# Kernel optimization log

Hardware: AMD Instinct MI355X
Metric: run time of the kernel (lower is better)

## Reference

```python
import jax, jax.numpy as jnp
import numpy as np

D = 256        # in_dim == out_dim for both node types
NH = 8         # n_heads
DH = D // NH   # d_over_h = 32
NA = 50000     # nodes of type 'a'
NB = 20000     # nodes of type 'b'
E = 100000     # edges per edge type
MAX_LEN = 27759
LN_EPS = 1e-5


def _rte_table():
    # Fixed (non-trainable) sinusoidal table from RelativeTemporalEncoding
    pos = np.arange(MAX_LEN, dtype=np.float32)[:, None]
    div = np.exp(np.arange(0, D, 2, dtype=np.float32) * (-np.log(10000.0) / D))
    tab = np.zeros((MAX_LEN, D), dtype=np.float32)
    tab[:, 0::2] = np.sin(pos * div) / np.sqrt(D)
    tab[:, 1::2] = np.cos(pos * div) / np.sqrt(D)
    return jnp.asarray(tab)


def setup_inputs() -> dict:
    key = jax.random.key(0)
    ks = jax.random.split(key, 24)
    s = 1.0 / np.sqrt(D)
    sh = 1.0 / np.sqrt(DH)
    inp = {
        "Ha": jax.random.normal(ks[0], (NA, D), jnp.float32),
        "Hb": jax.random.normal(ks[1], (NB, D), jnp.float32),
        "rte_emb": _rte_table(),
        # stacked per-node-type weights, index 0 -> 'a', 1 -> 'b'; torch Linear layout [out, in]
        "Wq": jax.random.normal(ks[2], (2, D, D), jnp.float32) * s,
        "Wk": jax.random.normal(ks[3], (2, D, D), jnp.float32) * s,
        "Wm": jax.random.normal(ks[4], (2, D, D), jnp.float32) * s,
        "Wa": jax.random.normal(ks[5], (2, D, D), jnp.float32) * s,
        "rteW": jax.random.normal(ks[6], (2, D, D), jnp.float32) * s,
        "rteb": jnp.zeros((2, D), jnp.float32),
        "ln_g": jnp.ones((2, D), jnp.float32),
        "ln_b": jnp.zeros((2, D), jnp.float32),
        "res_alpha": jnp.ones((2,), jnp.float32),
        # stacked per-edge-type params, index 0 -> e1 (a->a), 1 -> e2 (b->a), 2 -> e3 (a->b)
        "Watt": jax.random.normal(ks[7], (3, DH, DH), jnp.float32) * sh,
        "Wmsg": jax.random.normal(ks[8], (3, DH, DH), jnp.float32) * sh,
        "prior": jnp.ones((3,), jnp.float32),
        "src1": jax.random.randint(ks[9], (E,), 0, NA, jnp.int32),
        "dst1": jax.random.randint(ks[10], (E,), 0, NA, jnp.int32),
        "t1": jax.random.randint(ks[11], (E,), 1, MAX_LEN, jnp.int32),
        "src2": jax.random.randint(ks[12], (E,), 0, NB, jnp.int32),
        "dst2": jax.random.randint(ks[13], (E,), 0, NA, jnp.int32),
        "t2": jax.random.randint(ks[14], (E,), 1, MAX_LEN, jnp.int32),
        "src3": jax.random.randint(ks[15], (E,), 0, NA, jnp.int32),
        "dst3": jax.random.randint(ks[16], (E,), 0, NB, jnp.int32),
        "t3": jax.random.randint(ks[17], (E,), 1, MAX_LEN, jnp.int32),
    }
    return inp


def _edge_agg(Hs, Hd, src, dst, t, Wk_s, Wm_s, Wq_t, rW, rb, Wa_e, Wm_e, pr, rte_emb, n_dst):
    """Per-edge-type attention + segment softmax + weighted scatter-sum."""
    ne = src.shape[0]
    # RTE on gathered source features: h_src + Linear(emb[27759 - time])
    hs = Hs[src] + rte_emb[MAX_LEN - t] @ rW.T + rb            # [E, D]
    K = (hs @ Wk_s.T).reshape(ne, NH, DH)                       # [E, H, DH]
    Q = (Hd[dst] @ Wq_t.T).reshape(ne, NH, DH)                  # [E, H, DH]
    att = jnp.einsum('ehd,df,ehf->eh', K, Wa_e, Q) * pr / np.sqrt(DH).astype(np.float32)
    msg = jnp.einsum('ehd,df->ehf', (hs @ Wm_s.T).reshape(ne, NH, DH), Wm_e)
    # segment softmax over destination nodes (DGL mailbox softmax)
    amax = jax.lax.stop_gradient(jax.ops.segment_max(att, dst, num_segments=n_dst))
    ex = jnp.exp(att - amax[dst])
    den = jax.ops.segment_sum(ex, dst, num_segments=n_dst)
    w = ex / den[dst]                                           # [E, H]
    agg = jax.ops.segment_sum(w[..., None] * msg, dst, num_segments=n_dst)  # [N, H, DH]
    cnt = jax.ops.segment_sum(jnp.ones((ne,), jnp.float32), dst, num_segments=n_dst)
    return agg, (cnt > 0).astype(jnp.float32)


def _update(agg, Hx, Wa_n, g, b, ra):
    x = jax.nn.elu(agg.reshape(agg.shape[0], -1)) @ Wa_n.T
    alpha = jax.nn.sigmoid(ra)
    u = alpha * x + (1.0 - alpha) * Hx
    mu = jnp.mean(u, axis=-1, keepdims=True)
    var = jnp.var(u, axis=-1, keepdims=True)
    return (u - mu) / jnp.sqrt(var + LN_EPS) * g + b


def reference(Ha, Hb, rte_emb, Wq, Wk, Wm, Wa, rteW, rteb, ln_g, ln_b, res_alpha,
              Watt, Wmsg, prior, src1, dst1, t1, src2, dst2, t2, src3, dst3, t3):
    # e1: a -> a ; e2: b -> a ; e3: a -> b
    agg1, h1 = _edge_agg(Ha, Ha, src1, dst1, t1, Wk[0], Wm[0], Wq[0], rteW[0], rteb[0], Watt[0], Wmsg[0], prior[0], rte_emb, NA)
    agg2, h2 = _edge_agg(Hb, Ha, src2, dst2, t2, Wk[1], Wm[1], Wq[0], rteW[1], rteb[1], Watt[1], Wmsg[1], prior[1], rte_emb, NA)
    agg3, h3 = _edge_agg(Ha, Hb, src3, dst3, t3, Wk[0], Wm[0], Wq[1], rteW[0], rteb[0], Watt[2], Wmsg[2], prior[2], rte_emb, NB)
    # cross_reducer='mean': average over edge types that delivered messages
    agg_a = (agg1 + agg2) / jnp.maximum(h1 + h2, 1.0)[:, None, None]
    agg_b = agg3 / jnp.maximum(h3, 1.0)[:, None, None]
    out_a = _update(agg_a, Ha, Wa[0], ln_g[0], ln_b[0], res_alpha[0])
    out_b = _update(agg_b, Hb, Wa[1], ln_g[1], ln_b[1], res_alpha[1])
    return (out_a, out_b)
```

## Files before the change

kernel.cpp:

```cpp
#include <hip/hip_runtime.h>
#include <hip/hip_bf16.h>
#include <math.h>

typedef __hip_bfloat16 bf16;
typedef __attribute__((ext_vector_type(8))) short bf16x8v;
typedef __attribute__((ext_vector_type(4))) float f32x4;


__device__ __forceinline__ float eluf(float x) { return x > 0.f ? x : (__expf(x) - 1.f); }
__device__ __forceinline__ float b2f(unsigned short u) { return __uint_as_float((unsigned)u << 16); }
__device__ __forceinline__ unsigned short f2b(float f) {
    unsigned u = __float_as_uint(f);
    return (unsigned short)((u + 0x7fffu + ((u >> 16) & 1u)) >> 16);
}
__device__ __forceinline__ void unpack8(uint4 u, float* o) {
    o[0] = __uint_as_float(u.x << 16); o[1] = __uint_as_float(u.x & 0xffff0000u);
    o[2] = __uint_as_float(u.y << 16); o[3] = __uint_as_float(u.y & 0xffff0000u);
    o[4] = __uint_as_float(u.z << 16); o[5] = __uint_as_float(u.z & 0xffff0000u);
    o[6] = __uint_as_float(u.w << 16); o[7] = __uint_as_float(u.w & 0xffff0000u);
}
__device__ __forceinline__ void unpack4(ushort4 u, float* o) {
    o[0] = b2f(u.x); o[1] = b2f(u.y); o[2] = b2f(u.z); o[3] = b2f(u.w);
}

#define ASYNC_LDS16(g, l) \
    __builtin_amdgcn_global_load_lds((const __attribute__((address_space(1))) void*)(g), \
                                     (__attribute__((address_space(3))) void*)(l), 16, 0, 0)

__global__ void zero_kernel(int* __restrict__ z0, int nz0, int* __restrict__ z1, int nz1)
{
    for (int i = blockIdx.x * 256 + threadIdx.x; i < nz0; i += gridDim.x * 256) z0[i] = 0;
    if (blockIdx.x == 0 && threadIdx.x < (unsigned)nz1) z1[threadIdx.x] = 0;
}

__global__ void conv_fold_hist_kernel(
    const float* s0, bf16* o0, int n0, const float* s1, bf16* o1, int n1,
    const float* s2, bf16* o2, int n2, const float* s3, bf16* o3, int n3,
    const float* s4, bf16* o4, int n4, const float* s5, bf16* o5, int n5,
    const float* __restrict__ Watt, const float* __restrict__ Wmsg,
    const float* __restrict__ prior,
    const float* __restrict__ Wq, const float* __restrict__ Wm,
    bf16* __restrict__ WcatA, bf16* __restrict__ WcatB,
    float* __restrict__ Wmx1f, float* __restrict__ Wmx2f, float* __restrict__ Wmx3f,
    const int* __restrict__ d1, const int* __restrict__ d2, const int* __restrict__ d3,
    int2* __restrict__ m1, int2* __restrict__ m2, int2* __restrict__ m3,
    int E1, int E2, int E3)
{
    const int bid = blockIdx.x;
    if (bid < 3072) {
        const int seg = bid >> 9;
        const int lb = bid & 511;
        const float* sp; bf16* op; int n8;
        switch (seg) {
            case 0: sp = s0; op = o0; n8 = n0; break;
            case 1: sp = s1; op = o1; n8 = n1; break;
            case 2: sp = s2; op = o2; n8 = n2; break;
            case 3: sp = s3; op = o3; n8 = n3; break;
            case 4: sp = s4; op = o4; n8 = n4; break;
            default: sp = s5; op = o5; n8 = n5; break;
        }
        for (int i = lb * 256 + threadIdx.x; i < n8; i += 512 * 256) {
            const float4* p = (const float4*)(sp + (size_t)i * 8);
            float4 a = p[0], b = p[1];
            uint4 u;
            u.x = (unsigned)f2b(a.x) | ((unsigned)f2b(a.y) << 16);
            u.y = (unsigned)f2b(a.z) | ((unsigned)f2b(a.w) << 16);
            u.z = (unsigned)f2b(b.x) | ((unsigned)f2b(b.y) << 16);
            u.w = (unsigned)f2b(b.z) | ((unsigned)f2b(b.w) << 16);
            *(uint4*)(op + (size_t)i * 8) = u;
        }
        return;
    }
    if (bid >= 4608) {
        int i = (bid - 4608) * 256 + threadIdx.x;
        if (i < E1) atomicAdd(&m1[d1[i]].y, 1);
        else if (i < E1 + E2) atomicAdd(&m2[d2[i - E1]].y, 1);
        else if (i < E1 + E2 + E3) atomicAdd(&m3[d3[i - E1 - E2]].y, 1);
        return;
    }
    const int fb = bid - 3072;
    const int g = fb >> 8;
    const int i = fb & 255;
    const int j = threadIdx.x;
    const int h = i >> 5, r = i & 31;
    const float* A; const float* W; float sc = 1.f; int tr = 0;
    bf16* ob; float* of = nullptr;
    const float isq = 0.17677669529663687f;
    switch (g) {
        case 0: A = Watt;        sc = prior[0] * isq; W = Wq;         ob = WcatA;                       break;
        case 1: A = Watt + 1024; sc = prior[1] * isq; W = Wq;         ob = WcatA + (size_t)256 * 256;   break;
        case 2: A = Watt + 2048; sc = prior[2] * isq; W = Wq + 65536; ob = WcatB;                       break;
        case 3: A = Wmsg;        tr = 1; W = Wm;         ob = WcatA + (size_t)768 * 256;  of = Wmx1f;   break;
        case 4: A = Wmsg + 1024; tr = 1; W = Wm + 65536; ob = WcatB + (size_t)512 * 256;  of = Wmx2f;   break;
        default:A = Wmsg + 2048; tr = 1; W = Wm;         ob = WcatA + (size_t)1024 * 256; of = Wmx3f;   break;
    }
    __shared__ float arow[32];
    if (j < 32) arow[j] = (tr ? A[j * 32 + r] : A[r * 32 + j]) * sc;
    __syncthreads();
    float acc = 0.f;
    for (int k = 0; k < 32; ++k) acc += arow[k] * W[(size_t)(h * 32 + k) * 256 + j];
    ((unsigned short*)ob)[(size_t)i * 256 + j] = f2b(acc);
    if (of) of[(size_t)i * 256 + j] = acc;
}

__global__ void comb5alloc_kernel(const float* __restrict__ Wk,
                                  const float* __restrict__ Wmx1f, const float* __restrict__ Wmx2f,
                                  const float* __restrict__ Wmx3f,
                                  const float* __restrict__ rteW, const float* __restrict__ rteb,
                                  bf16* __restrict__ WcatR, float* __restrict__ bcatR,
                                  int2* __restrict__ meta, int* __restrict__ cursor,
                                  int* __restrict__ gtot, int NA, int NB, int bps)
{
    if (blockIdx.x >= 1280) {
        const int lid = (int)blockIdx.x - 1280;
        const int slot = lid / bps;
        const int base = (slot == 0) ? 0 : (slot == 1) ? NA : 2 * NA;
        const int len = (slot == 2) ? NB : NA;
        int i = (lid % bps) * 256 + threadIdx.x;
        if (i >= len) return;
        int* gp = gtot + slot;
        int idx = base + i;
        int s = atomicAdd(gp, meta[idx].y);
        meta[idx].x = s; cursor[idx] = s;
        return;
    }
    const int g = blockIdx.x >> 8;
    const int i = blockIdx.x & 255;
    const int j = threadIdx.x;
    const float* Wp; const float* rW; const float* rb; int op;
    switch (g) {
        case 0: Wp = Wk;         rW = rteW;         rb = rteb;       op = 0; break;
        case 1: Wp = Wk + 65536; rW = rteW + 65536; rb = rteb + 256; op = 2; break;
        case 2: Wp = Wmx1f;      rW = rteW;         rb = rteb;       op = 1; break;
        case 3: Wp = Wmx2f;      rW = rteW + 65536; rb = rteb + 256; op = 3; break;
        default:Wp = Wmx3f;      rW = rteW;         rb = rteb;       op = 4; break;
    }
    __shared__ float wrow[256];
    wrow[j] = Wp[i * 256 + j];
    __syncthreads();
    float acc = 0.f;
    for (int k = 0; k < 256; ++k) acc += wrow[k] * rW[k * 256 + j];
    ((unsigned short*)WcatR)[(size_t)(op * 256 + i) * 256 + j] = f2b(acc);
    if (j == 0) {
        float b = 0.f;
        for (int k = 0; k < 256; ++k) b += wrow[k] * rb[k];
        bcatR[op * 256 + i] = b;
    }
}

__device__ __forceinline__ void gemm_body(
    const bf16* __restrict__ A, const bf16* __restrict__ Wcat,
    const float* __restrict__ bcat,
    bf16* C0, bf16* C1, bf16* C2, bf16* C3, bf16* C4,
    int wideMask, int M, int bx, int by, char* As, char* Bs)
{
    const int tid = threadIdx.x;
    const int wid = tid >> 6, lane = tid & 63;
    const size_t row0 = (size_t)bx * 128;
    const int gcol0 = by * 128;
    const int cb = by >> 1;
    const int lcol0 = (by & 1) * 128;
    bf16* Csel = (cb == 0) ? C0 : (cb == 1) ? C1 : (cb == 2) ? C2 : (cb == 3) ? C3 : C4;
    const size_t cstride = ((wideMask >> cb) & 1) ? 512 : 256;
    const int wr = wid >> 1, wc = wid & 1;

    f32x4 zero = {0.f, 0.f, 0.f, 0.f};
    f32x4 acc[4][4];
#pragma unroll
    for (int m = 0; m < 4; ++m)
#pragma unroll
        for (int n = 0; n < 4; ++n) acc[m][n] = zero;

    const int sr = wid * 32 + (lane >> 3);
    const int scc = (lane & 7) << 4;
    const char* Ab = (const char*)A;
    const char* Wb = (const char*)Wcat;

    for (int k0 = 0; k0 < 512; k0 += 128) {
#pragma unroll
        for (int i = 0; i < 4; ++i) {
            const int r = sr + i * 8;
            const int csw = scc ^ ((r & 7) << 4);
            const int ldso = wid * 4096 + i * 1024;
            ASYNC_LDS16(Ab + (row0 + r) * 512 + k0 + csw, As + ldso);
            ASYNC_LDS16(Wb + (size_t)(gcol0 + r) * 512 + k0 + csw, Bs + ldso);
        }
        __syncthreads();
#pragma unroll
        for (int kk = 0; kk < 2; ++kk) {
            bf16x8v a[4], b[4];
            const int cbase = kk * 64 + ((lane >> 4) << 4);
#pragma unroll
            for (int m = 0; m < 4; ++m) {
                const int r = wr * 64 + m * 16 + (lane & 15);
                a[m] = *(const bf16x8v*)(As + r * 128 + (cbase ^ ((r & 7) << 4)));
            }
#pragma unroll
            for (int n = 0; n < 4; ++n) {
                const int r = wc * 64 + n * 16 + (lane & 15);
                b[n] = *(const bf16x8v*)(Bs + r * 128 + (cbase ^ ((r & 7) << 4)));
            }
#pragma unroll
            for (int m = 0; m < 4; ++m)
#pragma unroll
                for (int n = 0; n < 4; ++n)
                    acc[m][n] = __builtin_amdgcn_mfma_f32_16x16x32_bf16(a[m], b[n], acc[m][n], 0, 0, 0);
        }
        __syncthreads();
    }
    const int orow = (lane >> 4) << 2;
    const int ocol = lane & 15;
    float bv[4];
#pragma unroll
    for (int n = 0; n < 4; ++n)
        bv[n] = bcat ? bcat[gcol0 + wc * 64 + n * 16 + ocol] : 0.f;
    unsigned short* Cp = (unsigned short*)Csel;
#pragma unroll
    for (int m = 0; m < 4; ++m) {
#pragma unroll
        for (int j = 0; j < 4; ++j) {
            const size_t row = row0 + wr * 64 + m * 16 + orow + j;
            if ((int)row >= M) continue;
#pragma unroll
            for (int n = 0; n < 4; ++n) {
                const int col = lcol0 + wc * 64 + n * 16 + ocol;
                Cp[row * cstride + col] = f2b(acc[m][n][j] + bv[n]);
            }
        }
    }
}

__global__ __launch_bounds__(256) void gemm3s_kernel(
    const bf16* A0, const bf16* W0, const float* bc0,
    bf16* o00, bf16* o01, bf16* o02, bf16* o03, bf16* o04, int mask0, int M0,
    const bf16* A1, const bf16* W1,
    bf16* o10, bf16* o11, bf16* o12, bf16* o13, bf16* o14, int mask1, int M1,
    const bf16* A2, const bf16* W2,
    bf16* o20, bf16* o21, bf16* o22, int mask2, int M2,
    int b0, int b1, int btot,
    const int* __restrict__ d1, const int* __restrict__ d2, const int* __restrict__ d3,
    const int* __restrict__ s1, const int* __restrict__ s2, const int* __restrict__ s3,
    const int* __restrict__ tv1, const int* __restrict__ tv2, const int* __restrict__ tv3,
    int* __restrict__ cur1, int* __restrict__ cur2, int* __restrict__ cur3,
    int2* __restrict__ el1, int2* __restrict__ el2, int2* __restrict__ el3,
    int E1, int E2, int E3, int ml)
{
    __shared__ __align__(16) char As[16384];
    __shared__ __align__(16) char Bs[16384];
    const int bid = blockIdx.x;
    if (bid >= btot) {
        int i = (bid - btot) * 256 + threadIdx.x;
        if (i < E1) {
            int p = atomicAdd(&cur1[d1[i]], 1);
            el1[p] = make_int2(s1[i], ml - tv1[i]);
        } else if (i < E1 + E2) {
            int e = i - E1; int p = atomicAdd(&cur2[d2[e]], 1);
            el2[p] = make_int2(s2[e], ml - tv2[e]);
        } else if (i < E1 + E2 + E3) {
            int e = i - E1 - E2; int p = atomicAdd(&cur3[d3[e]], 1);
            el3[p] = make_int2(s3[e], ml - tv3[e]);
        }
        return;
    }
    if (bid < b0) {
        gemm_body(A0, W0, bc0, o00, o01, o02, o03, o04, mask0, M0,
                  bid / 10, bid % 10, As, Bs);
    } else if (bid < b1) {
        const int lid = bid - b0;
        gemm_body(A1, W1, nullptr, o10, o11, o12, o13, o14, mask1, M1,
                  lid / 10, lid % 10, As, Bs);
    } else {
        const int lid = bid - b1;
        gemm_body(A2, W2, nullptr, o20, o21, o22, o22, o22, mask2, M2,
                  lid / 6, lid % 6, As, Bs);
    }
}

__global__ __launch_bounds__(512) void ugemm_ln_kernel(
    const bf16* __restrict__ AG, const bf16* __restrict__ Wp,
    const bf16* __restrict__ Hbf, const float* __restrict__ g,
    const float* __restrict__ b, const float* __restrict__ ra,
    float* __restrict__ out, int M)
{
    __shared__ __align__(16) char As[16384];
    __shared__ __align__(16) char Bs[32768];
    __shared__ float red[128][8];
    const int tid = threadIdx.x;
    const int wid = tid >> 6, lane = tid & 63;
    const int wr = wid >> 2, wc = wid & 3;
    const size_t row0 = (size_t)blockIdx.x * 128;

    f32x4 zero = {0.f, 0.f, 0.f, 0.f};
    f32x4 acc[4][4];
#pragma unroll
    for (int m = 0; m < 4; ++m)
#pragma unroll
        for (int n = 0; n < 4; ++n) acc[m][n] = zero;

    const char* Ab = (const char*)AG;
    const char* Wb = (const char*)Wp;
    for (int k0 = 0; k0 < 512; k0 += 128) {
#pragma unroll
        for (int i = 0; i < 2; ++i) {
            const int r = wid * 16 + i * 8 + (lane >> 3);
            const int csw = ((lane & 7) << 4) ^ ((r & 7) << 4);
            ASYNC_LDS16(Ab + (row0 + r) * 512 + k0 + csw, As + (wid * 16 + i * 8) * 128);
        }
#pragma unroll
        for (int i = 0; i < 4; ++i) {
            const int r = wid * 32 + i * 8 + (lane >> 3);
            const int csw = ((lane & 7) << 4) ^ ((r & 7) << 4);
            ASYNC_LDS16(Wb + (size_t)r * 512 + k0 + csw, Bs + (wid * 32 + i * 8) * 128);
        }
        __syncthreads();
#pragma unroll
        for (int kk = 0; kk < 2; ++kk) {
            bf16x8v a[4], bv[4];
            const int cbase = kk * 64 + ((lane >> 4) << 4);
#pragma unroll
            for (int m = 0; m < 4; ++m) {
                const int r = wr * 64 + m * 16 + (lane & 15);
                a[m] = *(const bf16x8v*)(As + r * 128 + (cbase ^ ((r & 7) << 4)));
            }
#pragma unroll
            for (int n = 0; n < 4; ++n) {
                const int r = wc * 64 + n * 16 + (lane & 15);
                bv[n] = *(const bf16x8v*)(Bs + r * 128 + (cbase ^ ((r & 7) << 4)));
            }
#pragma unroll
            for (int m = 0; m < 4; ++m)
#pragma unroll
                for (int n = 0; n < 4; ++n)
                    acc[m][n] = __builtin_amdgcn_mfma_f32_16x16x32_bf16(a[m], bv[n], acc[m][n], 0, 0, 0);
        }
        __syncthreads();
    }
    const float alpha = 1.f / (1.f + __expf(-ra[0]));
    const float beta = 1.f - alpha;
    const int orow = (lane >> 4) << 2;
    const int ocol = lane & 15;
    float gv[4], bb[4];
#pragma unroll
    for (int n = 0; n < 4; ++n) {
        gv[n] = g[wc * 64 + n * 16 + ocol];
        bb[n] = b[wc * 64 + n * 16 + ocol];
    }
    const unsigned short* Hp = (const unsigned short*)Hbf;
#pragma unroll
    for (int m = 0; m < 4; ++m) {
#pragma unroll
        for (int j = 0; j < 4; ++j) {
            const int rl = wr * 64 + m * 16 + orow + j;
            const size_t grow = row0 + rl;
            float s = 0.f, s2 = 0.f;
#pragma unroll
            for (int n = 0; n < 4; ++n) {
                const int col = wc * 64 + n * 16 + ocol;
                float hv = ((int)grow < M) ? b2f(Hp[grow * 256 + col]) : 0.f;
                float u = alpha * acc[m][n][j] + beta * hv;
                acc[m][n][j] = u;
                s += u; s2 += u * u;
            }
            s += __shfl_xor(s, 1); s2 += __shfl_xor(s2, 1);
            s += __shfl_xor(s, 2); s2 += __shfl_xor(s2, 2);
            s += __shfl_xor(s, 4); s2 += __shfl_xor(s2, 4);
            s += __shfl_xor(s, 8); s2 += __shfl_xor(s2, 8);
            if (ocol == 0) { red[rl][wc] = s; red[rl][4 + wc] = s2; }
        }
    }
    __syncthreads();
#pragma unroll
    for (int m = 0; m < 4; ++m) {
#pragma unroll
        for (int j = 0; j < 4; ++j) {
            const int rl = wr * 64 + m * 16 + orow + j;
            const size_t grow = row0 + rl;
            if ((int)grow >= M) continue;
            float S = red[rl][0] + red[rl][1] + red[rl][2] + red[rl][3];
            float S2 = red[rl][4] + red[rl][5] + red[rl][6] + red[rl][7];
            const float mu = S * 0.00390625f;
            const float var = S2 * 0.00390625f - mu * mu;
            const float inv = rsqrtf(var + 1e-5f);
#pragma unroll
            for (int n = 0; n < 4; ++n) {
                const int col = wc * 64 + n * 16 + ocol;
                out[grow * 256 + col] = (acc[m][n][j] - mu) * inv * gv[n] + bb[n];
            }
        }
    }
}

__device__ __forceinline__ void epass16(
    const bf16* __restrict__ KM, const bf16* __restrict__ RKM,
    const int2* __restrict__ el, int beg, int num,
    int sx_l, int tt_l,
    const float q[8], int lane,
    float s[8], float& denOut)
{
    float den = 0.f;
    const char* KMb = (const char*)KM + lane * 16;
    const char* RMb = (const char*)RKM + lane * 16;
    auto edge = [&](uint4 km, uint4 rm) {
        float a[8], b[8];
        unpack8(km, a); unpack8(rm, b);
#pragma unroll
        for (int x = 0; x < 8; ++x) a[x] += b[x];
        float p = a[0] * q[0] + a[1] * q[1] + a[2] * q[2] + a[3] * q[3]
                + a[4] * q[4] + a[5] * q[5] + a[6] * q[6] + a[7] * q[7];
        p += __shfl_xor(p, 1); p += __shfl_xor(p, 2);
        float ex = __expf(p);
        float exb = __shfl_xor(ex, 32);
        den += exb;
#pragma unroll
        for (int x = 0; x < 8; ++x) s[x] += exb * a[x];
    };
    for (int c0 = 0; c0 < num; c0 += 64) {
        int nc = num - c0; if (nc > 64) nc = 64;
        if (c0 > 0) {
            sx_l = 0; tt_l = 0;
            if (lane < nc) { int2 e = el[beg + c0 + lane]; sx_l = e.x; tt_l = e.y; }
        }
        for (int i0 = 0; i0 < nc; i0 += 4) {
            const int rem = nc - i0;
            const int a0 = __shfl(sx_l, i0),     b0 = __shfl(tt_l, i0);
            const int a1 = __shfl(sx_l, i0 | 1), b1 = __shfl(tt_l, i0 | 1);
            const int a2 = __shfl(sx_l, i0 | 2), b2 = __shfl(tt_l, i0 | 2);
            const int a3 = __shfl(sx_l, i0 | 3), b3 = __shfl(tt_l, i0 | 3);
            uint4 km0, rm0, km1, rm1, km2, rm2, km3, rm3;
            km0 = *(const uint4*)(KMb + (size_t)a0 * 1024);
            rm0 = *(const uint4*)(RMb + (size_t)b0 * 1024);
            if (rem > 1) {
                km1 = *(const uint4*)(KMb + (size_t)a1 * 1024);
                rm1 = *(const uint4*)(RMb + (size_t)b1 * 1024);
            }
            if (rem > 2) {
                km2 = *(const uint4*)(KMb + (size_t)a2 * 1024);
                rm2 = *(const uint4*)(RMb + (size_t)b2 * 1024);
            }
            if (rem > 3) {
                km3 = *(const uint4*)(KMb + (size_t)a3 * 1024);
                rm3 = *(const uint4*)(RMb + (size_t)b3 * 1024);
            }
            edge(km0, rm0);
            if (rem > 1) edge(km1, rm1);
            if (rem > 2) edge(km2, rm2);
            if (rem > 3) edge(km3, rm3);
        }
    }
    denOut = den;
}

__device__ __forceinline__ void epass8(
    const bf16* __restrict__ Kh, const bf16* __restrict__ RKh,
    const bf16* __restrict__ Mt, const bf16* __restrict__ RMt,
    const int2* __restrict__ el, int beg, int num,
    int sx_l, int tt_l,
    const float q[4], int lane,
    float s[4], float& denOut)
{
    float den = 0.f;
    const char* Kb = (const char*)Kh + lane * 8;
    const char* Rb = (const char*)RKh + lane * 8;
    const char* Mb = (const char*)Mt + lane * 8;
    const char* Ub = (const char*)RMt + lane * 8;
    auto edge = [&](ushort4 kv, ushort4 rv, ushort4 mv, ushort4 uv) {
        float a[4], b[4], m[4], r[4];
        unpack4(kv, a); unpack4(rv, b); unpack4(mv, m); unpack4(uv, r);
        float p = (a[0] + b[0]) * q[0] + (a[1] + b[1]) * q[1]
                + (a[2] + b[2]) * q[2] + (a[3] + b[3]) * q[3];
        p += __shfl_xor(p, 1); p += __shfl_xor(p, 2); p += __shfl_xor(p, 4);
        float ex = __expf(p);
        den += ex;
#pragma unroll
        for (int x = 0; x < 4; ++x) s[x] += ex * (m[x] + r[x]);
    };
    for (int c0 = 0; c0 < num; c0 += 64) {
        int nc = num - c0; if (nc > 64) nc = 64;
        if (c0 > 0) {
            sx_l = 0; tt_l = 0;
            if (lane < nc) { int2 e = el[beg + c0 + lane]; sx_l = e.x; tt_l = e.y; }
        }
        for (int i0 = 0; i0 < nc; i0 += 4) {
            const int rem = nc - i0;
            const int a0 = __shfl(sx_l, i0),     b0 = __shfl(tt_l, i0);
            const int a1 = __shfl(sx_l, i0 | 1), b1 = __shfl(tt_l, i0 | 1);
            const int a2 = __shfl(sx_l, i0 | 2), b2 = __shfl(tt_l, i0 | 2);
            const int a3 = __shfl(sx_l, i0 | 3), b3 = __shfl(tt_l, i0 | 3);
            ushort4 k0, r0, m0, u0, k1, r1, m1, u1, k2, r2, m2, u2, k3, r3, m3, u3;
            k0 = *(const ushort4*)(Kb + (size_t)a0 * 1024);
            r0 = *(const ushort4*)(Rb + (size_t)b0 * 1024);
            m0 = *(const ushort4*)(Mb + (size_t)a0 * 512);
            u0 = *(const ushort4*)(Ub + (size_t)b0 * 512);
            if (rem > 1) {
                k1 = *(const ushort4*)(Kb + (size_t)a1 * 1024);
                r1 = *(const ushort4*)(Rb + (size_t)b1 * 1024);
                m1 = *(const ushort4*)(Mb + (size_t)a1 * 512);
                u1 = *(const ushort4*)(Ub + (size_t)b1 * 512);
            }
            if (rem > 2) {
                k2 = *(const ushort4*)(Kb + (size_t)a2 * 1024);
                r2 = *(const ushort4*)(Rb + (size_t)b2 * 1024);
                m2 = *(const ushort4*)(Mb + (size_t)a2 * 512);
                u2 = *(const ushort4*)(Ub + (size_t)b2 * 512);
            }
            if (rem > 3) {
                k3 = *(const ushort4*)(Kb + (size_t)a3 * 1024);
                r3 = *(const ushort4*)(Rb + (size_t)b3 * 1024);
                m3 = *(const ushort4*)(Mb + (size_t)a3 * 512);
                u3 = *(const ushort4*)(Ub + (size_t)b3 * 512);
            }
            edge(k0, r0, m0, u0);
            if (rem > 1) edge(k1, r1, m1, u1);
            if (rem > 2) edge(k2, r2, m2, u2);
            if (rem > 3) edge(k3, r3, m3, u3);
        }
    }
    denOut = den;
}

__global__ __launch_bounds__(256) void edge_fused_kernel(
    const bf16* __restrict__ Qa1, const bf16* __restrict__ Qa2,
    const bf16* __restrict__ KMa1, const bf16* __restrict__ RKM1,
    const int2* __restrict__ meta1, const int2* __restrict__ el1,
    const bf16* __restrict__ KMb, const bf16* __restrict__ RKM2,
    const int2* __restrict__ meta2, const int2* __restrict__ el2,
    bf16* __restrict__ AGa, int NA,
    const bf16* __restrict__ Qb3, const bf16* __restrict__ Ma3, const bf16* __restrict__ RM3p,
    const int2* __restrict__ meta3, const int2* __restrict__ el3,
    bf16* __restrict__ AGb, int NB, int nbblk)
{
    const int wid = threadIdx.x >> 6, lane = threadIdx.x & 63;
    if ((int)blockIdx.x >= nbblk) {
        const int n = ((int)blockIdx.x - nbblk) * 4 + wid;
        if (n >= NA) return;
        const int2 m1 = meta1[n], m2 = meta2[n];
        const int beg1 = m1.x, num1 = m1.y, beg2 = m2.x, num2 = m2.y;
        int sx1 = 0, tt1 = 0, sx2 = 0, tt2 = 0;
        if (lane < (num1 < 64 ? num1 : 64)) { int2 e = el1[beg1 + lane]; sx1 = e.x; tt1 = e.y; }
        if (lane < (num2 < 64 ? num2 : 64)) { int2 e = el2[beg2 + lane]; sx2 = e.x; tt2 = e.y; }
        float q1[8];
        unpack8(*(const uint4*)(Qa1 + (size_t)n * 256 + (lane & 31) * 8), q1);
        const uint4 qv2 = *(const uint4*)(Qa2 + (size_t)n * 256 + (lane & 31) * 8);
        float sf[8] = {0.f, 0.f, 0.f, 0.f, 0.f, 0.f, 0.f, 0.f};
        float s[8], den;
        if (num1 > 0) {
#pragma unroll
            for (int x = 0; x < 8; ++x) s[x] = 0.f;
            epass16(KMa1, RKM1, el1, beg1, num1, sx1, tt1, q1, lane, s, den);
            float invd = 1.f / den;
#pragma unroll
            for (int x = 0; x < 8; ++x) sf[x] += s[x] * invd;
        }
        if (num2 > 0) {
            float q2[8];
            unpack8(qv2, q2);
#pragma unroll
            for (int x = 0; x < 8; ++x) s[x] = 0.f;
            epass16(KMb, RKM2, el2, beg2, num2, sx2, tt2, q2, lane, s, den);
            float invd = 1.f / den;
#pragma unroll
            for (int x = 0; x < 8; ++x) sf[x] += s[x] * invd;
        }
        float dv = 1.f / fmaxf((float)((num1 > 0) + (num2 > 0)), 1.f);
        if (lane >= 32) {
            uint4 o;
            o.x = (unsigned)f2b(eluf(sf[0] * dv)) | ((unsigned)f2b(eluf(sf[1] * dv)) << 16);
            o.y = (unsigned)f2b(eluf(sf[2] * dv)) | ((unsigned)f2b(eluf(sf[3] * dv)) << 16);
            o.z = (unsigned)f2b(eluf(sf[4] * dv)) | ((unsigned)f2b(eluf(sf[5] * dv)) << 16);
            o.w = (unsigned)f2b(eluf(sf[6] * dv)) | ((unsigned)f2b(eluf(sf[7] * dv)) << 16);
            *(uint4*)((unsigned short*)AGa + (size_t)n * 256 + (lane - 32) * 8) = o;
        }
    } else {
        const int n = (int)blockIdx.x * 4 + wid;
        if (n >= NB) return;
        const int2 m3 = meta3[n];
        const int beg3 = m3.x, num3 = m3.y;
        int sx3 = 0, tt3 = 0;
        if (lane < (num3 < 64 ? num3 : 64)) { int2 e = el3[beg3 + lane]; sx3 = e.x; tt3 = e.y; }
        float q3[4];
        unpack4(*(const ushort4*)(Qb3 + (size_t)n * 256 + lane * 4), q3);
        float s[4] = {0.f, 0.f, 0.f, 0.f};
        float den = 1.f;
        if (num3 > 0) {
            epass8(KMa1, RKM1, Ma3, RM3p, el3, beg3, num3, sx3, tt3, q3, lane, s, den);
            float invd = 1.f / den;
#pragma unroll
            for (int x = 0; x < 4; ++x) s[x] *= invd;
        }
        ushort4 o;
        o.x = f2b(eluf(s[0])); o.y = f2b(eluf(s[1]));
        o.z = f2b(eluf(s[2])); o.w = f2b(eluf(s[3]));
        *(ushort4*)((unsigned short*)AGb + (size_t)n * 256 + lane * 4) = o;
    }
}

extern "C" void kernel_launch(void* const* d_in, const int* in_sizes, int n_in,
                              void* d_out, int out_size, void* d_ws, size_t ws_size,
                              hipStream_t stream)
{
    const float* Ha   = (const float*)d_in[0];
    const float* Hb   = (const float*)d_in[1];
    const float* rte  = (const float*)d_in[2];
    const float* Wq   = (const float*)d_in[3];
    const float* Wk   = (const float*)d_in[4];
    const float* Wm   = (const float*)d_in[5];
    const float* Wa   = (const float*)d_in[6];
    const float* rteW = (const float*)d_in[7];
    const float* rteb = (const float*)d_in[8];
    const float* ln_g = (const float*)d_in[9];
    const float* ln_b = (const float*)d_in[10];
    const float* ra   = (const float*)d_in[11];
    const float* Watt = (const float*)d_in[12];
    const float* Wmsg = (const float*)d_in[13];
    const float* prior= (const float*)d_in[14];
    const int* src1 = (const int*)d_in[15];
    const int* dst1 = (const int*)d_in[16];
    const int* t1   = (const int*)d_in[17];
    const int* src2 = (const int*)d_in[18];
    const int* dst2 = (const int*)d_in[19];
    const int* t2   = (const int*)d_in[20];
    const int* src3 = (const int*)d_in[21];
    const int* dst3 = (const int*)d_in[22];
    const int* t3   = (const int*)d_in[23];

    const int NA = in_sizes[0] / 256;
    const int NB = in_sizes[1] / 256;
    const int ML = in_sizes[2] / 256;
    const int E1 = in_sizes[15];
    const int E2 = in_sizes[18];
    const int E3 = in_sizes[21];
    const int NAp = (NA + 127) & ~127;
    const int NBp = (NB + 127) & ~127;
    const int MLp = (ML + 127) & ~127;

    char* w = (char*)d_ws;
    size_t off = 0;
    auto alloc = [&](size_t bytes) -> void* {
        void* p = w + off;
        off += (bytes + 511) & ~(size_t)511;
        return p;
    };
    bf16* WcatA = (bf16*)alloc((size_t)1280 * 256 * 2);
    bf16* WcatB = (bf16*)alloc((size_t)768 * 256 * 2);
    bf16* WcatR = (bf16*)alloc((size_t)1280 * 256 * 2);
    float* bcatR = (float*)alloc(1280 * 4);
    bf16* Wa_bf = (bf16*)alloc(131072 * 2);
    float* Wmx1f = (float*)alloc(65536 * 4);
    float* Wmx2f = (float*)alloc(65536 * 4);
    float* Wmx3f = (float*)alloc(65536 * 4);
    bf16* Ha_bf = (bf16*)alloc((size_t)NAp * 512);
    bf16* Hb_bf = (bf16*)alloc((size_t)NBp * 512);
    bf16* rte_bf = (bf16*)alloc((size_t)MLp * 512);
    bf16* Qa1 = (bf16*)alloc((size_t)NAp * 512);
    bf16* Qa2 = (bf16*)alloc((size_t)NAp * 512);
    bf16* KMa1 = (bf16*)alloc((size_t)NAp * 1024);
    bf16* RKM1 = (bf16*)alloc((size_t)MLp * 1024);
    bf16* RKM2 = (bf16*)alloc((size_t)MLp * 1024);
    bf16* RM3p = (bf16*)alloc((size_t)MLp * 512);
    int2* meta = (int2*)alloc((size_t)(NA + NA + NB) * 8);
    int2* meta1 = meta, *meta2 = meta + NA, *meta3 = meta + 2 * NA;
    int* curb = (int*)alloc((size_t)(NA + NA + NB) * 4);
    int* cur1 = curb, *cur2 = curb + NA, *cur3 = curb + 2 * NA;
    int2* elist1 = (int2*)alloc((size_t)E1 * 8);
    int2* elist2 = (int2*)alloc((size_t)E2 * 8);
    int2* elist3 = (int2*)alloc((size_t)E3 * 8);
    int* gtot = (int*)alloc(16);
    bf16* Ma3 = (bf16*)d_out;
    bf16* Qb3 = (bf16*)d_out + (size_t)NAp * 256;
    bf16* KMb = (bf16*)d_out + (size_t)NAp * 256 + (size_t)NBp * 256;
    bf16* AGa = Qa1;
    bf16* AGb = Qb3;

    const int Etot = E1 + E2 + E3;
    const int histB = (Etot + 255) / 256;
    const int bps = (((NA > NB ? NA : NB) + 255) / 256);

    zero_kernel<<<512, 256, 0, stream>>>((int*)meta, 2 * (NA + NA + NB), gtot, 4);

    conv_fold_hist_kernel<<<4608 + histB, 256, 0, stream>>>(
        Ha, Ha_bf, NA * 32, Hb, Hb_bf, NB * 32, rte, rte_bf, ML * 32,
        Wa, Wa_bf, 16384,
        Wk, WcatA + (size_t)512 * 256, 8192,
        Wk + 65536, WcatB + (size_t)256 * 256, 8192,
        Watt, Wmsg, prior, Wq, Wm, WcatA, WcatB, Wmx1f, Wmx2f, Wmx3f,
        dst1, dst2, dst3, meta1, meta2, meta3, E1, E2, E3);

    comb5alloc_kernel<<<1280 + bps * 3, 256, 0, stream>>>(
        Wk, Wmx1f, Wmx2f, Wmx3f, rteW, rteb, WcatR, bcatR,
        meta, curb, gtot, NA, NB, bps);

    const int nx0 = MLp / 128, nx1 = NAp / 128, nx2 = NBp / 128;
    const int b0 = nx0 * 10;
    const int b1 = b0 + nx1 * 10;
    const int btot = b1 + nx2 * 6;
    gemm3s_kernel<<<dim3(btot + histB), 256, 0, stream>>>(
        rte_bf, WcatR, bcatR, RKM1, RKM1 + 256, RKM2, RKM2 + 256, RM3p, 0xF, ML,
        Ha_bf, WcatA, Qa1, Qa2, KMa1, KMa1 + 256, Ma3, 0xC, NA,
        Hb_bf, WcatB, Qb3, KMb, KMb + 256, 0x6, NB,
        b0, b1, btot,
        dst1, dst2, dst3, src1, src2, src3, t1, t2, t3,
        cur1, cur2, cur3, elist1, elist2, elist3, E1, E2, E3, ML);

    const int nablk = (NA + 3) / 4;
    const int nbblk = (NB + 3) / 4;
    edge_fused_kernel<<<dim3(nablk + nbblk), 256, 0, stream>>>(
        Qa1, Qa2, KMa1, RKM1, meta1, elist1,
        KMb, RKM2, meta2, elist2,
        AGa, NA,
        Qb3, Ma3, RM3p, meta3, elist3,
        AGb, NB, nbblk);

    float* out = (float*)d_out;
    ugemm_ln_kernel<<<dim3(NBp / 128), 512, 0, stream>>>(
        AGb, Wa_bf + 65536, Hb_bf, ln_g + 256, ln_b + 256, ra + 1,
        out + (size_t)NA * 256, NB);
    ugemm_ln_kernel<<<dim3(NAp / 128), 512, 0, stream>>>(
        AGa, Wa_bf, Ha_bf, ln_g, ln_b, ra, out, NA);
}
```

Before: 347.6 us.

## Merge two update GEMM+LN launches and remap gemm blocks per XCD

Combines the two per-node-type update GEMM+LayerNorm launches into one grid, giving AGb its own buffer so the 'b' output no longer overwrites data the 'a' blocks read from d_out. This removes a launch and the tail between the two launches. It also remaps block IDs in the projection GEMM kernel so that consecutive logical tiles land on the same XCD, which should improve L2 reuse of shared A and W tiles. The cost is an extra scratch allocation and some index arithmetic per block.

```diff
diff --git a/kernel.cpp b/kernel.cpp
--- a/kernel.cpp
+++ b/kernel.cpp
@@ -262,33 +262,34 @@
         }
         return;
     }
-    if (bid < b0) {
+    const int q = btot >> 3, r = btot & 7;
+    const int xcd = bid & 7, idx = bid >> 3;
+    const int lbid = (xcd < r ? xcd * (q + 1) : r * (q + 1) + (xcd - r) * q) + idx;
+    if (lbid < b0) {
         gemm_body(A0, W0, bc0, o00, o01, o02, o03, o04, mask0, M0,
-                  bid / 10, bid % 10, As, Bs);
-    } else if (bid < b1) {
-        const int lid = bid - b0;
+                  lbid / 10, lbid % 10, As, Bs);
+    } else if (lbid < b1) {
+        const int lid = lbid - b0;
         gemm_body(A1, W1, nullptr, o10, o11, o12, o13, o14, mask1, M1,
                   lid / 10, lid % 10, As, Bs);
     } else {
-        const int lid = bid - b1;
+        const int lid = lbid - b1;
         gemm_body(A2, W2, nullptr, o20, o21, o22, o22, o22, mask2, M2,
                   lid / 6, lid % 6, As, Bs);
     }
 }
 
-__global__ __launch_bounds__(512) void ugemm_ln_kernel(
+__device__ __forceinline__ void ugemm_ln_body(
     const bf16* __restrict__ AG, const bf16* __restrict__ Wp,
     const bf16* __restrict__ Hbf, const float* __restrict__ g,
     const float* __restrict__ b, const float* __restrict__ ra,
-    float* __restrict__ out, int M)
-{
-    __shared__ __align__(16) char As[16384];
-    __shared__ __align__(16) char Bs[32768];
-    __shared__ float red[128][8];
+    float* __restrict__ out, int M, int bx,
+    char* As, char* Bs, float (*red)[8])
+{
     const int tid = threadIdx.x;
     const int wid = tid >> 6, lane = tid & 63;
     const int wr = wid >> 2, wc = wid & 3;
-    const size_t row0 = (size_t)blockIdx.x * 128;
+    const size_t row0 = (size_t)bx * 128;
 
     f32x4 zero = {0.f, 0.f, 0.f, 0.f};
     f32x4 acc[4][4];
@@ -387,6 +388,23 @@
                 out[grow * 256 + col] = (acc[m][n][j] - mu) * inv * gv[n] + bb[n];
             }
         }
+    }
+}
+
+__global__ __launch_bounds__(512) void ugemm2_ln_kernel(
+    const bf16* AGa, const bf16* Wpa, const bf16* Ha_bf, const float* ga,
+    const float* ba, const float* raa, float* outa, int Ma, int nba,
+    const bf16* AGb, const bf16* Wpb, const bf16* Hb_bf, const float* gb,
+    const float* bb, const float* rab, float* outb, int Mb)
+{
+    __shared__ __align__(16) char As[16384];
+    __shared__ __align__(16) char Bs[32768];
+    __shared__ float red[128][8];
+    const int bid = blockIdx.x;
+    if (bid < nba) {
+        ugemm_ln_body(AGa, Wpa, Ha_bf, ga, ba, raa, outa, Ma, bid, As, Bs, red);
+    } else {
+        ugemm_ln_body(AGb, Wpb, Hb_bf, gb, bb, rab, outb, Mb, bid - nba, As, Bs, red);
     }
 }
 
@@ -657,6 +675,7 @@
     bf16* RKM1 = (bf16*)alloc((size_t)MLp * 1024);
     bf16* RKM2 = (bf16*)alloc((size_t)MLp * 1024);
     bf16* RM3p = (bf16*)alloc((size_t)MLp * 512);
+    bf16* AGb = (bf16*)alloc((size_t)NBp * 512);
     int2* meta = (int2*)alloc((size_t)(NA + NA + NB) * 8);
     int2* meta1 = meta, *meta2 = meta + NA, *meta3 = meta + 2 * NA;
     int* curb = (int*)alloc((size_t)(NA + NA + NB) * 4);
@@ -669,7 +688,6 @@
     bf16* Qb3 = (bf16*)d_out + (size_t)NAp * 256;
     bf16* KMb = (bf16*)d_out + (size_t)NAp * 256 + (size_t)NBp * 256;
     bf16* AGa = Qa1;
-    bf16* AGb = Qb3;
 
     const int Etot = E1 + E2 + E3;
     const int histB = (Etot + 255) / 256;
@@ -711,9 +729,8 @@
         AGb, NB, nbblk);
 
     float* out = (float*)d_out;
-    ugemm_ln_kernel<<<dim3(NBp / 128), 512, 0, stream>>>(
+    ugemm2_ln_kernel<<<dim3(NAp / 128 + NBp / 128), 512, 0, stream>>>(
+        AGa, Wa_bf, Ha_bf, ln_g, ln_b, ra, out, NA, NAp / 128,
         AGb, Wa_bf + 65536, Hb_bf, ln_g + 256, ln_b + 256, ra + 1,
         out + (size_t)NA * 256, NB);
-    ugemm_ln_kernel<<<dim3(NAp / 128), 512, 0, stream>>>(
-        AGa, Wa_bf, Ha_bf, ln_g, ln_b, ra, out, NA);
-}
+}
```

Result: slower. 371.0 us (+6.7%).
